# Performance work log

Hardware: AMD Instinct MI355X
Metric: run time of the kernel (lower is better)

The kernel has to match this reference:

```python
import jax, jax.numpy as jnp
import numpy as np

B, S, D, H = 2, 2048, 1024, 16
HD = D // H  # head_dim = 64


def setup_inputs() -> dict:
    key = jax.random.key(0)
    ks = jax.random.split(key, 12)
    xav = (2.0 / (D + D)) ** 0.5  # xavier_normal std for square Linear
    q = jax.random.normal(ks[0], (B, S, D), jnp.float32)
    k = jax.random.normal(ks[1], (B, S, D), jnp.float32)
    v = jax.random.normal(ks[2], (B, S, D), jnp.float32)
    Wq = jax.random.normal(ks[3], (D, D), jnp.float32) * xav
    Wk = jax.random.normal(ks[4], (D, D), jnp.float32) * xav
    Wv = jax.random.normal(ks[5], (D, D), jnp.float32) * xav
    bq = jnp.zeros((D,), jnp.float32)
    bk = jnp.zeros((D,), jnp.float32)
    bv = jnp.zeros((D,), jnp.float32)
    # valid-prefix padding masks (True = valid token); key 0 always valid so
    # no causal softmax row is fully masked (avoids NaN, matches real usage).
    klen = jax.random.randint(ks[6], (B,), S // 2, S + 1)
    qlen = jax.random.randint(ks[7], (B,), S // 2, S + 1)
    pos = jnp.arange(S)
    key_padding_mask = pos[None, :] < klen[:, None]
    query_padding_mask = pos[None, :] < qlen[:, None]
    return {
        "q": q, "k": k, "v": v,
        "Wq": Wq, "bq": bq, "Wk": Wk, "bk": bk, "Wv": Wv, "bv": bv,
        "key_padding_mask": key_padding_mask,
        "query_padding_mask": query_padding_mask,
    }


def _proj_split(x, W, b, n_heads):
    # Linear (y = x W^T + b) then split heads: [B,S,D] -> [B,H,S,hd]
    bsz, sq, dm = x.shape
    hd = dm // n_heads
    y = x @ W.T + b
    return y.reshape(bsz, sq, n_heads, hd).transpose(0, 2, 1, 3)


def reference(q, k, v, Wq, bq, Wk, bk, Wv, bv, key_padding_mask, query_padding_mask):
    bsz, sq, dm = q.shape
    sk = k.shape[1]
    Q = _proj_split(q, Wq, bq, H)  # [B,H,Sq,hd]
    K = _proj_split(k, Wk, bk, H)  # [B,H,Sk,hd]
    V = _proj_split(v, Wv, bv, H)  # [B,H,Sk,hd]
    scale = 1.0 / jnp.sqrt(jnp.asarray(Q.shape[-1], Q.dtype))
    scores = jnp.einsum('bhqd,bhkd->bhqk', Q, K) * scale  # [B,H,Sq,Sk]
    # key padding: -inf where key invalid
    scores = jnp.where(key_padding_mask[:, None, None, :], scores, -jnp.inf)
    # causal: -inf strictly above the diagonal
    causal_ok = jnp.tril(jnp.ones((sq, sk), bool))
    scores = jnp.where(causal_ok[None, None, :, :], scores, -jnp.inf)
    attn = jax.nn.softmax(scores, axis=-1)
    # q_mask: zero out rows for padded queries (post-softmax, as in source)
    attn = jnp.where(query_padding_mask[:, None, :, None], attn, 0.0)
    # dropout p=0.0 -> identity
    out = jnp.einsum('bhqk,bhkd->bhqd', attn, V)
    out = out.transpose(0, 2, 1, 3).reshape(bsz, sq, dm)
    return out + q
```

## Files before the change

### kernel.cpp

```cpp
#include <hip/hip_runtime.h>
#include <stdint.h>

#define BATCH 2
#define SEQ 2048
#define DMODEL 1024
#define NHEAD 16
#define HDIM 64
#define CVT_BLOCKS 15360

typedef __attribute__((ext_vector_type(8))) short bf16x8;
typedef __attribute__((ext_vector_type(4))) float f32x4;

__device__ __forceinline__ unsigned short f2bf(float f) {
  unsigned int u = __float_as_uint(f);
  u += 0x7fffu + ((u >> 16) & 1u);
  return (unsigned short)(u >> 16);
}
__device__ __forceinline__ unsigned int pk2bf(float a, float b) {
  return __builtin_amdgcn_perm(__float_as_uint(b) + 0x8000u,
                               __float_as_uint(a) + 0x8000u, 0x07060302u);
}
__device__ __forceinline__ void async_copy16(const void* g, void* l) {
  __builtin_amdgcn_global_load_lds(
      (const __attribute__((address_space(1))) void*)g,
      (__attribute__((address_space(3))) void*)l, 16, 0, 0);
}

__global__ __launch_bounds__(256) void cvt_all(
    const float* __restrict__ q, const float* __restrict__ k,
    const float* __restrict__ v, const float* __restrict__ Wq,
    const float* __restrict__ Wk, const float* __restrict__ Wv,
    unsigned short* __restrict__ dst,
    const unsigned char* __restrict__ kp, const unsigned char* __restrict__ qp,
    int* __restrict__ lens) {
  if (blockIdx.x == CVT_BLOCKS) {
    const int t = threadIdx.x, wave = t >> 6, lane = t & 63;
    const unsigned char* base = (wave < 2) ? kp : qp;
    const int b = wave & 1;
    const bool bytefmt = (base[1] != 0);
    int cnt = 0;
    if (bytefmt) {
      const uint4* p = (const uint4*)(base + (size_t)b * SEQ);
#pragma unroll
      for (int g = 0; g < 2; g++) {
        const uint4 x = p[g * 64 + lane];
        const unsigned int w[4] = {x.x, x.y, x.z, x.w};
#pragma unroll
        for (int i = 0; i < 4; i++) {
          const unsigned int ww = w[i];
          cnt += ((ww & 0xffu) != 0) + ((ww & 0xff00u) != 0) +
                 ((ww & 0xff0000u) != 0) + ((ww & 0xff000000u) != 0);
        }
      }
    } else {
      const uint4* p = (const uint4*)(base + (size_t)b * SEQ * 4);
#pragma unroll
      for (int g = 0; g < 8; g++) {
        const uint4 x = p[g * 64 + lane];
        cnt += (x.x != 0) + (x.y != 0) + (x.z != 0) + (x.w != 0);
      }
    }
#pragma unroll
    for (int off = 32; off >= 1; off >>= 1) cnt += __shfl_xor(cnt, off, 64);
    if (lane == 0) lens[wave] = cnt;
    return;
  }
  const int g = blockIdx.x * 256 + threadIdx.x;
  const float* src;
  size_t off, dbase;
  if (g < 3 * (1 << 20)) {
    const int ti = g >> 20;
    src = (ti == 0) ? q : (ti == 1) ? k : v;
    off = (size_t)(g & ((1 << 20) - 1));
    dbase = (size_t)ti << 22;
  } else {
    const int gw = g - 3 * (1 << 20);
    const int ti = gw >> 18;
    src = (ti == 0) ? Wq : (ti == 1) ? Wk : Wv;
    off = (size_t)(gw & ((1 << 18) - 1));
    dbase = (3ull << 22) + ((size_t)ti << 20);
  }
  const float4 x = ((const float4*)src)[off];
  ushort4 o;
  o.x = f2bf(x.x); o.y = f2bf(x.y); o.z = f2bf(x.z); o.w = f2bf(x.w);
  *(ushort4*)(dst + dbase + off * 4) = o;
}

__global__ __launch_bounds__(256) void qkv_proj(
    const unsigned short* __restrict__ xq, const unsigned short* __restrict__ xk,
    const unsigned short* __restrict__ xv,
    const unsigned short* __restrict__ Wq, const float* __restrict__ bq,
    const unsigned short* __restrict__ Wk, const float* __restrict__ bk,
    const unsigned short* __restrict__ Wv, const float* __restrict__ bv,
    unsigned short* __restrict__ Qo, unsigned short* __restrict__ Ko,
    unsigned short* __restrict__ Vo, const int* __restrict__ lens) {
  const int z = blockIdx.z;
  const int m0 = blockIdx.y * 128, n0 = blockIdx.x * 128;
  const int b = m0 >> 11;
  const int len = (z == 0) ? lens[2 + b] : lens[b];
  if ((m0 & (SEQ - 1)) >= len) return;

  const unsigned short* x = (z == 0) ? xq : (z == 1) ? xk : xv;
  const unsigned short* W = (z == 0) ? Wq : (z == 1) ? Wk : Wv;
  const float* bias = (z == 0) ? bq : (z == 1) ? bk : bv;
  unsigned short* dst = (z == 0) ? Qo : (z == 1) ? Ko : Vo;
  const float osc = (z == 0) ? 0.18033688011112042f : 1.0f;

  __shared__ unsigned short As[128 * 64];
  __shared__ unsigned short Bs[128 * 64];

  const int t = threadIdx.x;
  const int wave = t >> 6, lane = t & 63, quad = lane >> 4, l16 = lane & 15;
  const int wm = wave >> 1, wn = wave & 1;

  const f32x4 fz = {0.f, 0.f, 0.f, 0.f};
  f32x4 acc[4][4];
#pragma unroll
  for (int i = 0; i < 4; i++)
#pragma unroll
    for (int j = 0; j < 4; j++) acc[i][j] = fz;

  for (int k0 = 0; k0 < DMODEL; k0 += 64) {
    __syncthreads();
#pragma unroll
    for (int c = 0; c < 4; c++) {
      const int slot = c * 256 + t;
      const int row = slot >> 3, pg = slot & 7;
      const int lg = (pg ^ (row & 7)) * 8;
      async_copy16(x + (size_t)(m0 + row) * DMODEL + k0 + lg,
                   (char*)As + (c * 256 + (t & 192)) * 16);
      async_copy16(W + (size_t)(n0 + row) * DMODEL + k0 + lg,
                   (char*)Bs + (c * 256 + (t & 192)) * 16);
    }
    __syncthreads();
#pragma unroll
    for (int kk = 0; kk < 2; kk++) {
      bf16x8 af[4], bfr[4];
#pragma unroll
      for (int i = 0; i < 4; i++) {
        const int ra = wm * 64 + i * 16 + l16;
        const int rb = wn * 64 + i * 16 + l16;
        af[i] = *(const bf16x8*)(As + ra * 64 + ((kk * 4 + quad) ^ (ra & 7)) * 8);
        bfr[i] = *(const bf16x8*)(Bs + rb * 64 + ((kk * 4 + quad) ^ (rb & 7)) * 8);
      }
      if (z == 2) {
#pragma unroll
        for (int i = 0; i < 4; i++)
#pragma unroll
          for (int j = 0; j < 4; j++)
            acc[i][j] = __builtin_amdgcn_mfma_f32_16x16x32_bf16(af[i], bfr[j], acc[i][j], 0, 0, 0);
      } else {
#pragma unroll
        for (int i = 0; i < 4; i++)
#pragma unroll
          for (int j = 0; j < 4; j++)
            acc[i][j] = __builtin_amdgcn_mfma_f32_16x16x32_bf16(bfr[j], af[i], acc[i][j], 0, 0, 0);
      }
    }
  }

  if (z == 2) {
#pragma unroll
    for (int j = 0; j < 4; j++) {
      const int n = n0 + wn * 64 + j * 16 + l16;
      const float bb_ = bias[n];
      const int h = n >> 6, hd = n & 63;
#pragma unroll
      for (int i = 0; i < 4; i++) {
        const int s0 = (m0 & (SEQ - 1)) + wm * 64 + i * 16 + quad * 4;
        uint2 w;
        w.x = pk2bf(acc[i][j][0] + bb_, acc[i][j][1] + bb_);
        w.y = pk2bf(acc[i][j][2] + bb_, acc[i][j][3] + bb_);
        *(uint2*)(dst + (((size_t)(b * NHEAD + h) * HDIM + hd) << 11) + s0) = w;
      }
    }
  } else {
#pragma unroll
    for (int j = 0; j < 4; j++) {
      const int nb = n0 + wn * 64 + j * 16 + quad * 4;
      const float4 b4 = *(const float4*)(bias + nb);
      const int h = nb >> 6, hd0 = nb & 63;
#pragma unroll
      for (int i = 0; i < 4; i++) {
        const int s = (m0 & (SEQ - 1)) + wm * 64 + i * 16 + l16;
        uint2 w;
        w.x = pk2bf((acc[i][j][0] + b4.x) * osc, (acc[i][j][1] + b4.y) * osc);
        w.y = pk2bf((acc[i][j][2] + b4.z) * osc, (acc[i][j][3] + b4.w) * osc);
        *(uint2*)(dst + (((size_t)(b * NHEAD + h) * SEQ + s) << 6) + hd0) = w;
      }
    }
  }
}


template <bool MASKED>
__device__ __forceinline__ void softmax_update(
    const f32x4 s[8], int key0, int qrow, int klen, int quad, int l16,
    float& mst, float& lsum, f32x4 o[4], unsigned short* Pdst) {
  float pm[8][4];
  float rm = -__builtin_inff();
  if (MASKED) {
    const int kmax = ((qrow < klen - 1) ? qrow : klen - 1) - key0 - quad * 4;
#pragma unroll
    for (int nf = 0; nf < 8; nf++)
#pragma unroll
      for (int r = 0; r < 4; r++) {
        pm[nf][r] = (nf * 16 + r <= kmax) ? s[nf][r] : -__builtin_inff();
        rm = fmaxf(rm, pm[nf][r]);
      }
  } else {
#pragma unroll
    for (int nf = 0; nf < 8; nf++)
#pragma unroll
      for (int r = 0; r < 4; r++) {
        pm[nf][r] = s[nf][r];
        rm = fmaxf(rm, pm[nf][r]);
      }
  }
  rm = fmaxf(rm, __shfl_xor(rm, 16, 64));
  rm = fmaxf(rm, __shfl_xor(rm, 32, 64));
  if (__ballot(rm > mst) != 0ull) {
    const float mnew = fmaxf(mst, rm);
    const float alpha = exp2f(fmaxf(mst, -1e30f) - fmaxf(mnew, -1e30f));
    mst = mnew;
    lsum *= alpha;
    float ab[4];
#pragma unroll
    for (int r = 0; r < 4; r++) ab[r] = __shfl(alpha, quad * 4 + r, 64);
#pragma unroll
    for (int db = 0; db < 4; db++)
#pragma unroll
      for (int r = 0; r < 4; r++) o[db][r] *= ab[r];
  }
  const float mref = fmaxf(mst, -1e30f);
  float rs = 0.f;
#pragma unroll
  for (int nf = 0; nf < 8; nf++)
#pragma unroll
    for (int r = 0; r < 4; r++) {
      const float p = exp2f(pm[nf][r] - mref);
      pm[nf][r] = p;
      rs += p;
    }
  rs += __shfl_xor(rs, 16, 64);
  rs += __shfl_xor(rs, 32, 64);
  lsum += rs;
#pragma unroll
  for (int nf = 0; nf < 8; nf++) {
    uint2 w;
    w.x = pk2bf(pm[nf][0], pm[nf][1]);
    w.y = pk2bf(pm[nf][2], pm[nf][3]);
    const int grp = (nf * 2 + (quad >> 1)) ^ l16;
    *(uint2*)(Pdst + l16 * 128 + grp * 8 + (quad & 1) * 4) = w;
  }
}

template <bool MASKED>
__device__ __forceinline__ void tile_pass(
    const unsigned short* __restrict__ ks, const unsigned short* __restrict__ vt,
    unsigned short* __restrict__ Pw, bf16x8 qf0, bf16x8 qf1,
    int key0, int qrow, int klen, int quad, int l16,
    float& mst, float& lsum, f32x4 o[4]) {
  const f32x4 fz = {0.f, 0.f, 0.f, 0.f};
  f32x4 s[8];
#pragma unroll
  for (int nf = 0; nf < 8; nf++) {
    const int row = nf * 16 + l16;
    const int sw = row & 7;
    const bf16x8 kf0 = *(const bf16x8*)(ks + row * 64 + (quad ^ sw) * 8);
    const bf16x8 kf1 = *(const bf16x8*)(ks + row * 64 + ((quad + 4) ^ sw) * 8);
    f32x4 a = fz;
    a = __builtin_amdgcn_mfma_f32_16x16x32_bf16(kf0, qf0, a, 0, 0, 0);
    a = __builtin_amdgcn_mfma_f32_16x16x32_bf16(kf1, qf1, a, 0, 0, 0);
    s[nf] = a;
  }
  softmax_update<MASKED>(s, key0, qrow, klen, quad, l16, mst, lsum, o, Pw);
  bf16x8 pf[4];
#pragma unroll
  for (int ksn = 0; ksn < 4; ksn++)
    pf[ksn] = *(const bf16x8*)(Pw + l16 * 128 + ((ksn * 4 + quad) ^ l16) * 8);
#pragma unroll
  for (int db = 0; db < 4; db++) {
    const int d = db * 16 + l16;
#pragma unroll
    for (int ksn = 0; ksn < 4; ksn++) {
      const bf16x8 v = *(const bf16x8*)(vt + d * 128 + ((ksn * 4 + quad) ^ l16) * 8);
      o[db] = __builtin_amdgcn_mfma_f32_16x16x32_bf16(pf[ksn], v, o[db], 0, 0, 0);
    }
  }
}

__global__ __launch_bounds__(256, 3) void attn_kernel(
    const unsigned short* __restrict__ Qb, const unsigned short* __restrict__ Kb,
    const unsigned short* __restrict__ VTb, const float* __restrict__ qin,
    const int* __restrict__ lens, float* __restrict__ out) {
  const int pi = blockIdx.x, h = blockIdx.y, b = blockIdx.z;
  const int lo = pi, hi = 31 - pi;
  const int bh = b * NHEAD + h;
  const int t = threadIdx.x, wave = t >> 6, lane = t & 63, quad = lane >> 4, l16 = lane & 15;
  const int klen = lens[b], qlen = lens[2 + b];
  const bool doHI = (hi * 64 < qlen);

  __shared__ unsigned short Ks[128 * 64];
  __shared__ unsigned short VT[64 * 128];
  __shared__ unsigned short Ps[4][16 * 128];

  const unsigned short* Qp = Qb + (size_t)bh * SEQ * HDIM;
  const unsigned short* Kp = Kb + (size_t)bh * SEQ * HDIM;
  const unsigned short* Vt = VTb + (size_t)bh * HDIM * SEQ;

  const int qrLO = lo * 64 + wave * 16 + l16;
  const int qrHI = hi * 64 + wave * 16 + l16;
  const bf16x8 qlo0 = *(const bf16x8*)(Qp + (size_t)qrLO * HDIM + quad * 8);
  const bf16x8 qlo1 = *(const bf16x8*)(Qp + (size_t)qrLO * HDIM + 32 + quad * 8);
  const bf16x8 qhi0 = *(const bf16x8*)(Qp + (size_t)qrHI * HDIM + quad * 8);
  const bf16x8 qhi1 = *(const bf16x8*)(Qp + (size_t)qrHI * HDIM + 32 + quad * 8);

  const f32x4 fz = {0.f, 0.f, 0.f, 0.f};
  f32x4 oLO[4], oHI[4];
#pragma unroll
  for (int i = 0; i < 4; i++) { oLO[i] = fz; oHI[i] = fz; }
  float mLO = -__builtin_inff(), lLO = 0.f;
  float mHI = -__builtin_inff(), lHI = 0.f;

  const int kendLO = ((lo * 64 + 64) < klen) ? (lo * 64 + 64) : klen;
  const int ktotLO = (kendLO + 127) >> 7;
  int ktotHI = 0;
  if (doHI) {
    const int kendHI = ((hi * 64 + 64) < klen) ? (hi * 64 + 64) : klen;
    ktotHI = (kendHI + 127) >> 7;
  }
  const int ktot = (ktotHI > ktotLO) ? ktotHI : ktotLO;

  for (int kt = 0; kt < ktot; kt++) {
    const int key0 = kt << 7;
    __syncthreads();
#pragma unroll
    for (int c = 0; c < 4; c++) {
      const int slot = c * 256 + t;
      const int row = slot >> 3, pg = slot & 7;
      async_copy16(Kp + (size_t)(key0 + row) * HDIM + (pg ^ (row & 7)) * 8,
                   (char*)Ks + (c * 256 + (t & 192)) * 16);
    }
#pragma unroll
    for (int c = 0; c < 4; c++) {
      const int slot = c * 256 + t;
      const int row = slot >> 4, pg = slot & 15;
      async_copy16(Vt + (size_t)row * SEQ + key0 + (pg ^ (row & 15)) * 8,
                   (char*)VT + (c * 256 + (t & 192)) * 16);
    }
    __syncthreads();

    if (kt < ktotHI) {
      if ((key0 + 127 <= hi * 64) && (key0 + 127 < klen))
        tile_pass<false>(Ks, VT, Ps[wave], qhi0, qhi1, key0, qrHI, klen, quad, l16, mHI, lHI, oHI);
      else
        tile_pass<true>(Ks, VT, Ps[wave], qhi0, qhi1, key0, qrHI, klen, quad, l16, mHI, lHI, oHI);
    }
    if (kt < ktotLO) {
      if ((key0 + 127 <= lo * 64) && (key0 + 127 < klen))
        tile_pass<false>(Ks, VT, Ps[wave], qlo0, qlo1, key0, qrLO, klen, quad, l16, mLO, lLO, oLO);
      else
        tile_pass<true>(Ks, VT, Ps[wave], qlo0, qlo1, key0, qrLO, klen, quad, l16, mLO, lLO, oLO);
    }
  }

  const float invLO = (lLO > 0.f) ? 1.f / lLO : 0.f;
  const float invHI = (lHI > 0.f) ? 1.f / lHI : 0.f;
  float ibLO[4], ibHI[4];
#pragma unroll
  for (int r = 0; r < 4; r++) {
    ibLO[r] = __shfl(invLO, quad * 4 + r, 64);
    ibHI[r] = __shfl(invHI, quad * 4 + r, 64);
  }
#pragma unroll
  for (int db = 0; db < 4; db++) {
    const int col = h * HDIM + db * 16 + l16;
#pragma unroll
    for (int r = 0; r < 4; r++) {
      const int iL = lo * 64 + wave * 16 + quad * 4 + r;
      const int iH = hi * 64 + wave * 16 + quad * 4 + r;
      const size_t oL = (size_t)(b * SEQ + iL) * DMODEL + col;
      const size_t oH = (size_t)(b * SEQ + iH) * DMODEL + col;
      out[oL] = ((iL < qlen) ? oLO[db][r] * ibLO[r] : 0.f) + qin[oL];
      out[oH] = ((iH < qlen) ? oHI[db][r] * ibHI[r] : 0.f) + qin[oH];
    }
  }
}

extern "C" void kernel_launch(void* const* d_in, const int* in_sizes, int n_in,
                              void* d_out, int out_size, void* d_ws, size_t ws_size,
                              hipStream_t stream) {
  (void)in_sizes; (void)n_in; (void)out_size; (void)ws_size;
  const float* q = (const float*)d_in[0];
  const float* k = (const float*)d_in[1];
  const float* v = (const float*)d_in[2];
  const float* Wq = (const float*)d_in[3];
  const float* bq = (const float*)d_in[4];
  const float* Wk = (const float*)d_in[5];
  const float* bk = (const float*)d_in[6];
  const float* Wv = (const float*)d_in[7];
  const float* bv = (const float*)d_in[8];
  const unsigned char* kpm = (const unsigned char*)d_in[9];
  const unsigned char* qpm = (const unsigned char*)d_in[10];
  float* out = (float*)d_out;

  const size_t tsz = (size_t)BATCH * SEQ * DMODEL;
  const size_t wsz = (size_t)DMODEL * DMODEL;

  char* ws = (char*)d_ws;
  int* lens = (int*)ws;
  unsigned short* cvt_base = (unsigned short*)(ws + 256);
  unsigned short* qb16 = cvt_base;
  unsigned short* kb16 = qb16 + tsz;
  unsigned short* vb16 = kb16 + tsz;
  unsigned short* Wqb = vb16 + tsz;
  unsigned short* Wkb = Wqb + wsz;
  unsigned short* Wvb = Wkb + wsz;
  unsigned short* Qw = Wvb + wsz;
  unsigned short* Kw = Qw + tsz;
  unsigned short* Vtw = Kw + tsz;

  cvt_all<<<dim3(CVT_BLOCKS + 1), dim3(256), 0, stream>>>(q, k, v, Wq, Wk, Wv,
                                                          cvt_base, kpm, qpm, lens);
  qkv_proj<<<dim3(8, 32, 3), dim3(256), 0, stream>>>(qb16, kb16, vb16, Wqb, bq, Wkb, bk, Wvb, bv, Qw, Kw, Vtw, lens);
  attn_kernel<<<dim3(16, NHEAD, BATCH), dim3(256), 0, stream>>>(Qw, Kw, Vtw, q, lens, out);
}
```

Baseline: 209.9 us.

## Split lo/hi query tiles across two wave groups in 512-thread attention blocks

The attention kernel now uses 512 threads per block. The first four waves process the low query tile and the last four process the paired high tile in parallel, where previously the same four waves processed both tiles in sequence. The K/V tile loads are shared across the 8 waves, with fewer copies per thread. This doubles the wave count per block to raise latency hiding and cut per-wave serial work, but the lo-group waves sit idle once their shorter causal range ends, and LDS use grows with the larger P buffer.

```diff
diff --git a/kernel.cpp b/kernel.cpp
--- a/kernel.cpp
+++ b/kernel.cpp
@@ -290,100 +290,85 @@
   }
 }
 
-__global__ __launch_bounds__(256, 3) void attn_kernel(
+__global__ __launch_bounds__(512, 4) void attn_kernel(
     const unsigned short* __restrict__ Qb, const unsigned short* __restrict__ Kb,
     const unsigned short* __restrict__ VTb, const float* __restrict__ qin,
     const int* __restrict__ lens, float* __restrict__ out) {
   const int pi = blockIdx.x, h = blockIdx.y, b = blockIdx.z;
-  const int lo = pi, hi = 31 - pi;
   const int bh = b * NHEAD + h;
   const int t = threadIdx.x, wave = t >> 6, lane = t & 63, quad = lane >> 4, l16 = lane & 15;
+  const int grp = wave >> 2, w4 = wave & 3;
+  const int lo = pi, hi = 31 - pi;
+  const int myTile = grp ? hi : lo;
   const int klen = lens[b], qlen = lens[2 + b];
-  const bool doHI = (hi * 64 < qlen);
 
   __shared__ unsigned short Ks[128 * 64];
   __shared__ unsigned short VT[64 * 128];
-  __shared__ unsigned short Ps[4][16 * 128];
+  __shared__ unsigned short Ps[8][16 * 128];
 
   const unsigned short* Qp = Qb + (size_t)bh * SEQ * HDIM;
   const unsigned short* Kp = Kb + (size_t)bh * SEQ * HDIM;
   const unsigned short* Vt = VTb + (size_t)bh * HDIM * SEQ;
 
-  const int qrLO = lo * 64 + wave * 16 + l16;
-  const int qrHI = hi * 64 + wave * 16 + l16;
-  const bf16x8 qlo0 = *(const bf16x8*)(Qp + (size_t)qrLO * HDIM + quad * 8);
-  const bf16x8 qlo1 = *(const bf16x8*)(Qp + (size_t)qrLO * HDIM + 32 + quad * 8);
-  const bf16x8 qhi0 = *(const bf16x8*)(Qp + (size_t)qrHI * HDIM + quad * 8);
-  const bf16x8 qhi1 = *(const bf16x8*)(Qp + (size_t)qrHI * HDIM + 32 + quad * 8);
+  const int qrow = myTile * 64 + w4 * 16 + l16;
+  const bf16x8 qf0 = *(const bf16x8*)(Qp + (size_t)qrow * HDIM + quad * 8);
+  const bf16x8 qf1 = *(const bf16x8*)(Qp + (size_t)qrow * HDIM + 32 + quad * 8);
 
   const f32x4 fz = {0.f, 0.f, 0.f, 0.f};
-  f32x4 oLO[4], oHI[4];
-#pragma unroll
-  for (int i = 0; i < 4; i++) { oLO[i] = fz; oHI[i] = fz; }
-  float mLO = -__builtin_inff(), lLO = 0.f;
-  float mHI = -__builtin_inff(), lHI = 0.f;
+  f32x4 o[4];
+#pragma unroll
+  for (int i = 0; i < 4; i++) o[i] = fz;
+  float mst = -__builtin_inff(), lsum = 0.f;
 
   const int kendLO = ((lo * 64 + 64) < klen) ? (lo * 64 + 64) : klen;
   const int ktotLO = (kendLO + 127) >> 7;
   int ktotHI = 0;
-  if (doHI) {
+  if (hi * 64 < qlen) {
     const int kendHI = ((hi * 64 + 64) < klen) ? (hi * 64 + 64) : klen;
     ktotHI = (kendHI + 127) >> 7;
   }
   const int ktot = (ktotHI > ktotLO) ? ktotHI : ktotLO;
+  const int myktot = grp ? ktotHI : ktotLO;
 
   for (int kt = 0; kt < ktot; kt++) {
     const int key0 = kt << 7;
     __syncthreads();
 #pragma unroll
-    for (int c = 0; c < 4; c++) {
-      const int slot = c * 256 + t;
+    for (int c = 0; c < 2; c++) {
+      const int slot = c * 512 + t;
       const int row = slot >> 3, pg = slot & 7;
       async_copy16(Kp + (size_t)(key0 + row) * HDIM + (pg ^ (row & 7)) * 8,
-                   (char*)Ks + (c * 256 + (t & 192)) * 16);
-    }
-#pragma unroll
-    for (int c = 0; c < 4; c++) {
-      const int slot = c * 256 + t;
+                   (char*)Ks + (c * 512 + (t & 448)) * 16);
+    }
+#pragma unroll
+    for (int c = 0; c < 2; c++) {
+      const int slot = c * 512 + t;
       const int row = slot >> 4, pg = slot & 15;
       async_copy16(Vt + (size_t)row * SEQ + key0 + (pg ^ (row & 15)) * 8,
-                   (char*)VT + (c * 256 + (t & 192)) * 16);
+                   (char*)VT + (c * 512 + (t & 448)) * 16);
     }
     __syncthreads();
 
-    if (kt < ktotHI) {
-      if ((key0 + 127 <= hi * 64) && (key0 + 127 < klen))
-        tile_pass<false>(Ks, VT, Ps[wave], qhi0, qhi1, key0, qrHI, klen, quad, l16, mHI, lHI, oHI);
+    if (kt < myktot) {
+      if ((key0 + 127 <= myTile * 64) && (key0 + 127 < klen))
+        tile_pass<false>(Ks, VT, Ps[wave], qf0, qf1, key0, qrow, klen, quad, l16, mst, lsum, o);
       else
-        tile_pass<true>(Ks, VT, Ps[wave], qhi0, qhi1, key0, qrHI, klen, quad, l16, mHI, lHI, oHI);
-    }
-    if (kt < ktotLO) {
-      if ((key0 + 127 <= lo * 64) && (key0 + 127 < klen))
-        tile_pass<false>(Ks, VT, Ps[wave], qlo0, qlo1, key0, qrLO, klen, quad, l16, mLO, lLO, oLO);
-      else
-        tile_pass<true>(Ks, VT, Ps[wave], qlo0, qlo1, key0, qrLO, klen, quad, l16, mLO, lLO, oLO);
-    }
-  }
-
-  const float invLO = (lLO > 0.f) ? 1.f / lLO : 0.f;
-  const float invHI = (lHI > 0.f) ? 1.f / lHI : 0.f;
-  float ibLO[4], ibHI[4];
-#pragma unroll
-  for (int r = 0; r < 4; r++) {
-    ibLO[r] = __shfl(invLO, quad * 4 + r, 64);
-    ibHI[r] = __shfl(invHI, quad * 4 + r, 64);
-  }
+        tile_pass<true>(Ks, VT, Ps[wave], qf0, qf1, key0, qrow, klen, quad, l16, mst, lsum, o);
+    }
+  }
+
+  const float inv = (lsum > 0.f) ? 1.f / lsum : 0.f;
+  float ib[4];
+#pragma unroll
+  for (int r = 0; r < 4; r++) ib[r] = __shfl(inv, quad * 4 + r, 64);
 #pragma unroll
   for (int db = 0; db < 4; db++) {
     const int col = h * HDIM + db * 16 + l16;
 #pragma unroll
     for (int r = 0; r < 4; r++) {
-      const int iL = lo * 64 + wave * 16 + quad * 4 + r;
-      const int iH = hi * 64 + wave * 16 + quad * 4 + r;
-      const size_t oL = (size_t)(b * SEQ + iL) * DMODEL + col;
-      const size_t oH = (size_t)(b * SEQ + iH) * DMODEL + col;
-      out[oL] = ((iL < qlen) ? oLO[db][r] * ibLO[r] : 0.f) + qin[oL];
-      out[oH] = ((iH < qlen) ? oHI[db][r] * ibHI[r] : 0.f) + qin[oH];
+      const int i = myTile * 64 + w4 * 16 + quad * 4 + r;
+      const size_t oo = (size_t)(b * SEQ + i) * DMODEL + col;
+      out[oo] = ((i < qlen) ? o[db][r] * ib[r] : 0.f) + qin[oo];
     }
   }
 }
@@ -424,5 +409,5 @@
   cvt_all<<<dim3(CVT_BLOCKS + 1), dim3(256), 0, stream>>>(q, k, v, Wq, Wk, Wv,
                                                           cvt_base, kpm, qpm, lens);
   qkv_proj<<<dim3(8, 32, 3), dim3(256), 0, stream>>>(qb16, kb16, vb16, Wqb, bq, Wkb, bk, Wvb, bv, Qw, Kw, Vtw, lens);
-  attn_kernel<<<dim3(16, NHEAD, BATCH), dim3(256), 0, stream>>>(Qw, Kw, Vtw, q, lens, out);
-}
+  attn_kernel<<<dim3(16, NHEAD, BATCH), dim3(512), 0, stream>>>(Qw, Kw, Vtw, q, lens, out);
+}
```

After: 210.0 us. About the same (+0.0%).

## Pair adjacent query tiles per block and fuse their K/V passes

Applied to the files above, without the earlier changes.

Each block now handles two adjacent 64-row query tiles (2p, 2p+1) instead of a low/high causal pair. A new tile_pass2 shares the K and V fragment loads from LDS across both tiles and interleaves their MFMAs. The tile assignment is rotated by head and reversed for batch 1 to balance work across blocks. This drops the symmetric lo/hi causal load balancing, so per-block work now varies widely, and the doubled score registers may increase register pressure.

```diff
diff --git a/kernel.cpp b/kernel.cpp
--- a/kernel.cpp
+++ b/kernel.cpp
@@ -290,16 +290,63 @@
   }
 }
 
+template <bool MASKED>
+__device__ __forceinline__ void tile_pass2(
+    const unsigned short* __restrict__ ks, const unsigned short* __restrict__ vt,
+    unsigned short* __restrict__ Pw,
+    bf16x8 qa0, bf16x8 qa1, bf16x8 qb0, bf16x8 qb1,
+    int key0, int qrA, int qrB, int klen, int quad, int l16,
+    float& mA, float& lA, f32x4 oA[4],
+    float& mB, float& lB, f32x4 oB[4]) {
+  const f32x4 fz = {0.f, 0.f, 0.f, 0.f};
+  f32x4 sA[8], sB[8];
+#pragma unroll
+  for (int nf = 0; nf < 8; nf++) {
+    const int row = nf * 16 + l16;
+    const int sw = row & 7;
+    const bf16x8 kf0 = *(const bf16x8*)(ks + row * 64 + (quad ^ sw) * 8);
+    const bf16x8 kf1 = *(const bf16x8*)(ks + row * 64 + ((quad + 4) ^ sw) * 8);
+    f32x4 a = fz, bb = fz;
+    a = __builtin_amdgcn_mfma_f32_16x16x32_bf16(kf0, qa0, a, 0, 0, 0);
+    a = __builtin_amdgcn_mfma_f32_16x16x32_bf16(kf1, qa1, a, 0, 0, 0);
+    bb = __builtin_amdgcn_mfma_f32_16x16x32_bf16(kf0, qb0, bb, 0, 0, 0);
+    bb = __builtin_amdgcn_mfma_f32_16x16x32_bf16(kf1, qb1, bb, 0, 0, 0);
+    sA[nf] = a;
+    sB[nf] = bb;
+  }
+  softmax_update<MASKED>(sA, key0, qrA, klen, quad, l16, mA, lA, oA, Pw);
+  bf16x8 pfA[4];
+#pragma unroll
+  for (int ksn = 0; ksn < 4; ksn++)
+    pfA[ksn] = *(const bf16x8*)(Pw + l16 * 128 + ((ksn * 4 + quad) ^ l16) * 8);
+  softmax_update<MASKED>(sB, key0, qrB, klen, quad, l16, mB, lB, oB, Pw);
+  bf16x8 pfB[4];
+#pragma unroll
+  for (int ksn = 0; ksn < 4; ksn++)
+    pfB[ksn] = *(const bf16x8*)(Pw + l16 * 128 + ((ksn * 4 + quad) ^ l16) * 8);
+#pragma unroll
+  for (int db = 0; db < 4; db++) {
+    const int d = db * 16 + l16;
+#pragma unroll
+    for (int ksn = 0; ksn < 4; ksn++) {
+      const bf16x8 v = *(const bf16x8*)(vt + d * 128 + ((ksn * 4 + quad) ^ l16) * 8);
+      oA[db] = __builtin_amdgcn_mfma_f32_16x16x32_bf16(pfA[ksn], v, oA[db], 0, 0, 0);
+      oB[db] = __builtin_amdgcn_mfma_f32_16x16x32_bf16(pfB[ksn], v, oB[db], 0, 0, 0);
+    }
+  }
+}
+
 __global__ __launch_bounds__(256, 3) void attn_kernel(
     const unsigned short* __restrict__ Qb, const unsigned short* __restrict__ Kb,
     const unsigned short* __restrict__ VTb, const float* __restrict__ qin,
     const int* __restrict__ lens, float* __restrict__ out) {
   const int pi = blockIdx.x, h = blockIdx.y, b = blockIdx.z;
-  const int lo = pi, hi = 31 - pi;
+  const int x = (pi + h) & 15;
+  const int p = b ? (15 - x) : x;
+  const int tA = 2 * p, tB = 2 * p + 1;
   const int bh = b * NHEAD + h;
   const int t = threadIdx.x, wave = t >> 6, lane = t & 63, quad = lane >> 4, l16 = lane & 15;
   const int klen = lens[b], qlen = lens[2 + b];
-  const bool doHI = (hi * 64 < qlen);
 
   __shared__ unsigned short Ks[128 * 64];
   __shared__ unsigned short VT[64 * 128];
@@ -309,28 +356,25 @@
   const unsigned short* Kp = Kb + (size_t)bh * SEQ * HDIM;
   const unsigned short* Vt = VTb + (size_t)bh * HDIM * SEQ;
 
-  const int qrLO = lo * 64 + wave * 16 + l16;
-  const int qrHI = hi * 64 + wave * 16 + l16;
-  const bf16x8 qlo0 = *(const bf16x8*)(Qp + (size_t)qrLO * HDIM + quad * 8);
-  const bf16x8 qlo1 = *(const bf16x8*)(Qp + (size_t)qrLO * HDIM + 32 + quad * 8);
-  const bf16x8 qhi0 = *(const bf16x8*)(Qp + (size_t)qrHI * HDIM + quad * 8);
-  const bf16x8 qhi1 = *(const bf16x8*)(Qp + (size_t)qrHI * HDIM + 32 + quad * 8);
+  const int qrA = tA * 64 + wave * 16 + l16;
+  const int qrB = tB * 64 + wave * 16 + l16;
+  const bf16x8 qa0 = *(const bf16x8*)(Qp + (size_t)qrA * HDIM + quad * 8);
+  const bf16x8 qa1 = *(const bf16x8*)(Qp + (size_t)qrA * HDIM + 32 + quad * 8);
+  const bf16x8 qb0 = *(const bf16x8*)(Qp + (size_t)qrB * HDIM + quad * 8);
+  const bf16x8 qb1 = *(const bf16x8*)(Qp + (size_t)qrB * HDIM + 32 + quad * 8);
 
   const f32x4 fz = {0.f, 0.f, 0.f, 0.f};
-  f32x4 oLO[4], oHI[4];
-#pragma unroll
-  for (int i = 0; i < 4; i++) { oLO[i] = fz; oHI[i] = fz; }
-  float mLO = -__builtin_inff(), lLO = 0.f;
-  float mHI = -__builtin_inff(), lHI = 0.f;
-
-  const int kendLO = ((lo * 64 + 64) < klen) ? (lo * 64 + 64) : klen;
-  const int ktotLO = (kendLO + 127) >> 7;
-  int ktotHI = 0;
-  if (doHI) {
-    const int kendHI = ((hi * 64 + 64) < klen) ? (hi * 64 + 64) : klen;
-    ktotHI = (kendHI + 127) >> 7;
-  }
-  const int ktot = (ktotHI > ktotLO) ? ktotHI : ktotLO;
+  f32x4 oA[4], oB[4];
+#pragma unroll
+  for (int i = 0; i < 4; i++) { oA[i] = fz; oB[i] = fz; }
+  float mA = -__builtin_inff(), lA = 0.f;
+  float mB = -__builtin_inff(), lB = 0.f;
+
+  const int kendA = ((tA * 64 + 64) < klen) ? (tA * 64 + 64) : klen;
+  const int kendB = ((tB * 64 + 64) < klen) ? (tB * 64 + 64) : klen;
+  const int ktA = (tA * 64 < qlen) ? ((kendA + 127) >> 7) : 0;
+  const int ktB = (tB * 64 < qlen) ? ((kendB + 127) >> 7) : 0;
+  const int ktot = (ktA > ktB) ? ktA : ktB;
 
   for (int kt = 0; kt < ktot; kt++) {
     const int key0 = kt << 7;
@@ -351,39 +395,48 @@
     }
     __syncthreads();
 
-    if (kt < ktotHI) {
-      if ((key0 + 127 <= hi * 64) && (key0 + 127 < klen))
-        tile_pass<false>(Ks, VT, Ps[wave], qhi0, qhi1, key0, qrHI, klen, quad, l16, mHI, lHI, oHI);
+    const bool aA = kt < ktA, aB = kt < ktB;
+    const bool mskB = !((key0 + 127 <= tB * 64) && (key0 + 127 < klen));
+    const bool mskA = !((key0 + 127 <= tA * 64) && (key0 + 127 < klen));
+    if (aA && aB) {
+      if (!mskA && !mskB)
+        tile_pass2<false>(Ks, VT, Ps[wave], qa0, qa1, qb0, qb1, key0, qrA, qrB,
+                          klen, quad, l16, mA, lA, oA, mB, lB, oB);
       else
-        tile_pass<true>(Ks, VT, Ps[wave], qhi0, qhi1, key0, qrHI, klen, quad, l16, mHI, lHI, oHI);
-    }
-    if (kt < ktotLO) {
-      if ((key0 + 127 <= lo * 64) && (key0 + 127 < klen))
-        tile_pass<false>(Ks, VT, Ps[wave], qlo0, qlo1, key0, qrLO, klen, quad, l16, mLO, lLO, oLO);
+        tile_pass2<true>(Ks, VT, Ps[wave], qa0, qa1, qb0, qb1, key0, qrA, qrB,
+                         klen, quad, l16, mA, lA, oA, mB, lB, oB);
+    } else if (aB) {
+      if (!mskB)
+        tile_pass<false>(Ks, VT, Ps[wave], qb0, qb1, key0, qrB, klen, quad, l16, mB, lB, oB);
       else
-        tile_pass<true>(Ks, VT, Ps[wave], qlo0, qlo1, key0, qrLO, klen, quad, l16, mLO, lLO, oLO);
-    }
-  }
-
-  const float invLO = (lLO > 0.f) ? 1.f / lLO : 0.f;
-  const float invHI = (lHI > 0.f) ? 1.f / lHI : 0.f;
-  float ibLO[4], ibHI[4];
+        tile_pass<true>(Ks, VT, Ps[wave], qb0, qb1, key0, qrB, klen, quad, l16, mB, lB, oB);
+    } else if (aA) {
+      if (!mskA)
+        tile_pass<false>(Ks, VT, Ps[wave], qa0, qa1, key0, qrA, klen, quad, l16, mA, lA, oA);
+      else
+        tile_pass<true>(Ks, VT, Ps[wave], qa0, qa1, key0, qrA, klen, quad, l16, mA, lA, oA);
+    }
+  }
+
+  const float invA = (lA > 0.f) ? 1.f / lA : 0.f;
+  const float invB = (lB > 0.f) ? 1.f / lB : 0.f;
+  float ibA[4], ibB[4];
 #pragma unroll
   for (int r = 0; r < 4; r++) {
-    ibLO[r] = __shfl(invLO, quad * 4 + r, 64);
-    ibHI[r] = __shfl(invHI, quad * 4 + r, 64);
+    ibA[r] = __shfl(invA, quad * 4 + r, 64);
+    ibB[r] = __shfl(invB, quad * 4 + r, 64);
   }
 #pragma unroll
   for (int db = 0; db < 4; db++) {
     const int col = h * HDIM + db * 16 + l16;
 #pragma unroll
     for (int r = 0; r < 4; r++) {
-      const int iL = lo * 64 + wave * 16 + quad * 4 + r;
-      const int iH = hi * 64 + wave * 16 + quad * 4 + r;
-      const size_t oL = (size_t)(b * SEQ + iL) * DMODEL + col;
-      const size_t oH = (size_t)(b * SEQ + iH) * DMODEL + col;
-      out[oL] = ((iL < qlen) ? oLO[db][r] * ibLO[r] : 0.f) + qin[oL];
-      out[oH] = ((iH < qlen) ? oHI[db][r] * ibHI[r] : 0.f) + qin[oH];
+      const int iA = tA * 64 + wave * 16 + quad * 4 + r;
+      const int iB = tB * 64 + wave * 16 + quad * 4 + r;
+      const size_t oa = (size_t)(b * SEQ + iA) * DMODEL + col;
+      const size_t ob = (size_t)(b * SEQ + iB) * DMODEL + col;
+      out[oa] = ((iA < qlen) ? oA[db][r] * ibA[r] : 0.f) + qin[oa];
+      out[ob] = ((iB < qlen) ? oB[db][r] * ibB[r] : 0.f) + qin[ob];
     }
   }
 }
```

Result: slower. 231.4 us (+10.3%).
